# Performance work log

Hardware: AMD Instinct MI355X
Metric: run time of the kernel (lower is better)

Reference implementation:

```python
import jax, jax.numpy as jnp
import numpy as np
from jax import lax

V, E, H, K, T, B = 32000, 512, 512, 32, 256, 64
PAD_W = 0          # word_dict['PAD']
START, END, PAD_L = 30, 31, 0   # label_dict
NEG = -100000.0


def setup_inputs() -> dict:
    key = jax.random.key(0)
    ks = jax.random.split(key, 12)
    s = 1.0 / np.sqrt(H)
    tokens = jax.random.randint(ks[0], (T, B), 1, V, dtype=jnp.int32)   # >PAD_W -> mask all ones
    tags = jax.random.randint(ks[1], (T, B), 1, K - 2, dtype=jnp.int32)
    lengths = jnp.full((B,), T, dtype=jnp.int32)
    embed = jax.random.normal(ks[2], (V, E), jnp.float32) * 0.1
    wih0 = jax.random.uniform(ks[3], (2, 4 * H, E), jnp.float32, -s, s)
    whh0 = jax.random.uniform(ks[4], (2, 4 * H, H), jnp.float32, -s, s)
    b0 = jax.random.uniform(ks[5], (2, 4 * H), jnp.float32, -s, s)
    wih1 = jax.random.uniform(ks[6], (2, 4 * H, 2 * H), jnp.float32, -s, s)
    whh1 = jax.random.uniform(ks[7], (2, 4 * H, H), jnp.float32, -s, s)
    b1 = jax.random.uniform(ks[8], (2, 4 * H), jnp.float32, -s, s)
    lin_w = jax.random.uniform(ks[9], (K, 2 * H), jnp.float32, -s, s)
    lin_b = jax.random.uniform(ks[10], (K,), jnp.float32, -s, s)
    trans = jax.random.normal(ks[11], (K, K), jnp.float32)
    # replicate the torch transition init (same order of assignments)
    trans = trans.at[START, :].set(NEG)
    trans = trans.at[:, END].set(NEG)
    trans = trans.at[:, PAD_L].set(NEG)
    trans = trans.at[PAD_L, :].set(NEG)
    trans = trans.at[PAD_L, END].set(0.0)
    trans = trans.at[PAD_L, PAD_L].set(0.0)
    return dict(tokens=tokens, tags=tags, lengths=lengths, embed=embed,
                wih0=wih0, whh0=whh0, b0=b0, wih1=wih1, whh1=whh1, b1=b1,
                lin_w=lin_w, lin_b=lin_b, trans=trans)


def _lstm_dir(x, w_ih, w_hh, b, reverse):
    # x: [T,B,in] -> hs: [T,B,H]; gates precomputed as one big GEMM
    xp = jnp.einsum('tbi,gi->tbg', x, w_ih) + b  # [T,B,4H]
    h0 = jnp.zeros((x.shape[1], H), x.dtype)

    def step(carry, g_in):
        h, c = carry
        g = g_in + h @ w_hh.T
        i, f, gg, o = jnp.split(g, 4, axis=-1)  # torch gate order i,f,g,o
        c = jax.nn.sigmoid(f) * c + jax.nn.sigmoid(i) * jnp.tanh(gg)
        h = jax.nn.sigmoid(o) * jnp.tanh(c)
        return (h, c), h

    _, hs = lax.scan(step, (h0, h0), xp, reverse=reverse)
    return hs


def _bilstm_layer(x, wih, whh, b):
    return jnp.concatenate([_lstm_dir(x, wih[0], whh[0], b[0], False),
                            _lstm_dir(x, wih[1], whh[1], b[1], True)], axis=-1)


def reference(tokens, tags, lengths, embed, wih0, whh0, b0, wih1, whh1, b1,
              lin_w, lin_b, trans):
    mask = (tokens > PAD_W).astype(jnp.float32)  # [T,B]
    x = embed[tokens]                            # [T,B,E]
    x = _bilstm_layer(x, wih0, whh0, b0)
    x = _bilstm_layer(x, wih1, whh1, b1)
    feats = x @ lin_w.T + lin_b                  # [T,B,K]

    nB = tokens.shape[1]
    # ---- CRF forward algorithm: log Z(x) ----
    init = jnp.full((nB, K), NEG, feats.dtype).at[:, START].set(0.0)

    def step(score, inp):
        emit, m = inp  # [B,K], [B]
        # new[b,k] = logsumexp_j(score[b,j] + trans[k,j]) + emit[b,k]
        new = jax.nn.logsumexp(score[:, None, :] + trans[None, :, :], axis=2) + emit
        return jnp.where(m[:, None] > 0, new, score), None

    z, _ = lax.scan(step, init, (feats, mask))
    log_z = jax.nn.logsumexp(z + trans[END][None, :], axis=1)  # [B]

    # ---- gold path score (vectorized, masked deltas sum) ----
    start_row = jnp.full((1, nB), START, dtype=tags.dtype)
    te = jnp.concatenate([start_row, tags], axis=0)            # [T+1,B]
    trans_s = trans[te[1:], te[:-1]]                           # [T,B]
    emit_s = jnp.take_along_axis(feats, te[1:][..., None].astype(jnp.int32), axis=2)[..., 0]
    gold = jnp.sum(mask * (trans_s + emit_s), axis=0) + trans[END, te[-1]]

    return jnp.sum((log_z - gold) / lengths.astype(jnp.float32))
```

## Files before the change

kernel.cpp:

```cpp
#include <hip/hip_runtime.h>
#include <math.h>

#define T_STEPS 256
#define BATCH   64
#define HID     512
#define KTAGS   32
#define NEGV    -100000.0f
#define START_TAG 30
#define END_TAG   31

#define NBLK      256
#define SPIN_LIM  (1 << 26)
#define LAYER_DONE  300u
#define POISON_DONE 301u
#define POISON    0xFFFFFFFFFFFFFFFFULL

typedef __attribute__((ext_vector_type(8))) short short8;
typedef __attribute__((ext_vector_type(4))) float f32x4;

union V16 { uint4 u; short8 s; };
union HQ  { unsigned long long q[2]; short8 s; };

static __device__ __forceinline__ unsigned short f2b(float f) {
    unsigned u = __float_as_uint(f);
    return (unsigned short)((u + 0x7fffu + ((u >> 16) & 1u)) >> 16);
}
static __device__ __forceinline__ float b2f(unsigned short us) {
    return __uint_as_float(((unsigned)us) << 16);
}

__global__ __launch_bounds__(256) void init_zero(unsigned int* __restrict__ flags,
                                                 unsigned long long* __restrict__ hbuf,
                                                 float* __restrict__ out)
{
    int i = blockIdx.x * 256 + threadIdx.x;
    if (i < 131072)
        __hip_atomic_store(hbuf + i, POISON, __ATOMIC_RELAXED, __HIP_MEMORY_SCOPE_AGENT);
    if (i < 16384)
        __hip_atomic_store(flags + i, 0u, __ATOMIC_RELAXED, __HIP_MEMORY_SCOPE_AGENT);
    if (i == 0)
        __hip_atomic_store(out, 0.0f, __ATOMIC_RELAXED, __HIP_MEMORY_SCOPE_AGENT);
}

__global__ __launch_bounds__(256) void convert_embed(const float* __restrict__ src,
                                                     unsigned short* __restrict__ dst)
{
    long long i = ((long long)blockIdx.x * 256 + threadIdx.x) * 4;
    if (i >= (long long)32000 * 512) return;
    float4 v = *(const float4*)(src + i);
    ushort4 o;
    o.x = f2b(v.x); o.y = f2b(v.y); o.z = f2b(v.z); o.w = f2b(v.w);
    *(ushort4*)(dst + i) = o;
}

__global__ __launch_bounds__(256) void pack_w(const float* __restrict__ wih,
                                              const float* __restrict__ whh,
                                              int xK,
                                              unsigned short* __restrict__ wpack)
{
    const int xKt = xK >> 5, KT = xKt + 16;
    long long t = (long long)blockIdx.x * 256 + threadIdx.x;
    if (t >= (long long)2 * 64 * KT * 2 * 64) return;
    int lane = (int)(t & 63);
    long long rest = t >> 6;
    int nf = (int)(rest & 1); rest >>= 1;
    int kt = (int)(rest % KT); rest /= KT;
    int nt = (int)(rest % 64);
    int d  = (int)(rest / 64);
    int c = lane & 15, q = lane >> 4;
    int bc = nf * 16 + c;
    int r = (bc >> 3) * 512 + nt * 8 + (bc & 7);
    const float* src;
    if (kt < xKt) src = wih + ((long long)d * 2048 * xK + (long long)r * xK + kt * 32 + q * 8);
    else          src = whh + ((long long)d * 2048 * 512 + (long long)r * 512 + (kt - xKt) * 32 + q * 8);
    float4 v0 = *(const float4*)src;
    float4 v1 = *(const float4*)(src + 4);
    unsigned short o[8] = { f2b(v0.x), f2b(v0.y), f2b(v0.z), f2b(v0.w),
                            f2b(v1.x), f2b(v1.y), f2b(v1.z), f2b(v1.w) };
    *(uint4*)(wpack + t * 8) = *(const uint4*)o;
}

template<int XK>
static __device__ __forceinline__ void layer_steps(
    const int d, const int bg, const int nt, const int tid,
    const int* __restrict__ tokens,
    const unsigned short* __restrict__ embB,
    const unsigned short* __restrict__ hs_in,
    const unsigned short* __restrict__ wp,
    const float* __restrict__ bia,
    unsigned short* __restrict__ hso,
    unsigned long long* __restrict__ hbuf64,
    uint4* __restrict__ wldsH,
    float (&Gred)[4][32][33],
    int* __restrict__ tok_s)
{
    constexpr bool L0  = (XK == 512);
    constexpr int  xKt = XK >> 5;
    constexpr int  nX  = xKt >> 2;

    const int w = tid >> 6, lane = tid & 63;
    const int lm = lane & 15, q = lane >> 4;
    const int brow = tid >> 3, hc = tid & 7;

    const uint4* wp4 = (const uint4*)wp;
    for (int j = tid; j < 2048; j += 256)
        wldsH[j] = wp4[xKt * 128 + j];

    float breg[4];
    #pragma unroll
    for (int g = 0; g < 4; ++g) breg[g] = bia[g * 512 + nt * 8 + hc];
    float creg = 0.0f;

    __syncthreads();

    for (int s = 0; s < T_STEPS; ++s) {
        const int tt = d ? (T_STEPS - 1 - s) : s;

        if (L0 && tid < 32) tok_s[tid] = tokens[tt * BATCH + bg * 32 + tid];
        __syncthreads();

        const unsigned short* xr[2];
        #pragma unroll
        for (int mt = 0; mt < 2; ++mt) {
            int m = mt * 16 + lm;
            if (L0) xr[mt] = embB + (long long)tok_s[m] * 512;
            else    xr[mt] = hs_in + ((long long)tt * 64 + bg * 32 + m) * 1024;
        }

        uint4 av[nX][2], bv[nX][2];
        #pragma unroll
        for (int i = 0; i < nX; ++i) {
            const int kt = w * nX + i;
            #pragma unroll
            for (int mt = 0; mt < 2; ++mt)
                av[i][mt] = *(const uint4*)(xr[mt] + kt * 32 + q * 8);
            #pragma unroll
            for (int nf = 0; nf < 2; ++nf)
                bv[i][nf] = *(const uint4*)(wp + ((long long)kt * 128 + nf * 64 + lane) * 8);
        }

        HQ hq[4][2];
        const unsigned long long* hbq =
            hbuf64 + (long long)(((((s - 1) & 7) * 2 + d) * 2 + bg)) * 4096;
        if (s > 0) {
            #pragma unroll
            for (int i = 0; i < 4; ++i) {
                const int kth = w * 4 + i;
                #pragma unroll
                for (int mt = 0; mt < 2; ++mt) {
                    const int base = (kth * 4 + q) * 64 + (mt * 16 + lm) * 2;
                    hq[i][mt].q[0] = __hip_atomic_load(hbq + base,     __ATOMIC_RELAXED, __HIP_MEMORY_SCOPE_AGENT);
                    hq[i][mt].q[1] = __hip_atomic_load(hbq + base + 1, __ATOMIC_RELAXED, __HIP_MEMORY_SCOPE_AGENT);
                }
            }
        }

        f32x4 acc[2][2];
        #pragma unroll
        for (int mt = 0; mt < 2; ++mt)
            #pragma unroll
            for (int nf = 0; nf < 2; ++nf) acc[mt][nf] = (f32x4)0.0f;

        #pragma unroll
        for (int i = 0; i < nX; ++i) {
            V16 a0, a1, b0, b1;
            a0.u = av[i][0]; a1.u = av[i][1];
            b0.u = bv[i][0]; b1.u = bv[i][1];
            acc[0][0] = __builtin_amdgcn_mfma_f32_16x16x32_bf16(a0.s, b0.s, acc[0][0], 0, 0, 0);
            acc[0][1] = __builtin_amdgcn_mfma_f32_16x16x32_bf16(a0.s, b1.s, acc[0][1], 0, 0, 0);
            acc[1][0] = __builtin_amdgcn_mfma_f32_16x16x32_bf16(a1.s, b0.s, acc[1][0], 0, 0, 0);
            acc[1][1] = __builtin_amdgcn_mfma_f32_16x16x32_bf16(a1.s, b1.s, acc[1][1], 0, 0, 0);
        }

        if (s > 0) {
            int n = 0;
            for (;;) {
                int bad = 0;
                #pragma unroll
                for (int i = 0; i < 4; ++i) {
                    const int kth = w * 4 + i;
                    #pragma unroll
                    for (int mt = 0; mt < 2; ++mt) {
                        const int base = (kth * 4 + q) * 64 + (mt * 16 + lm) * 2;
                        if (hq[i][mt].q[0] == POISON) {
                            hq[i][mt].q[0] = __hip_atomic_load(hbq + base,     __ATOMIC_RELAXED, __HIP_MEMORY_SCOPE_AGENT);
                            bad = 1;
                        }
                        if (hq[i][mt].q[1] == POISON) {
                            hq[i][mt].q[1] = __hip_atomic_load(hbq + base + 1, __ATOMIC_RELAXED, __HIP_MEMORY_SCOPE_AGENT);
                            bad = 1;
                        }
                    }
                }
                if (!bad) break;
                __builtin_amdgcn_s_sleep(1);
                if (++n > SPIN_LIM) break;
            }

            #pragma unroll
            for (int i = 0; i < 4; ++i) {
                const int kth = w * 4 + i;
                V16 b0, b1;
                b0.u = wldsH[(kth * 2 + 0) * 64 + lane];
                b1.u = wldsH[(kth * 2 + 1) * 64 + lane];
                acc[0][0] = __builtin_amdgcn_mfma_f32_16x16x32_bf16(hq[i][0].s, b0.s, acc[0][0], 0, 0, 0);
                acc[0][1] = __builtin_amdgcn_mfma_f32_16x16x32_bf16(hq[i][0].s, b1.s, acc[0][1], 0, 0, 0);
                acc[1][0] = __builtin_amdgcn_mfma_f32_16x16x32_bf16(hq[i][1].s, b0.s, acc[1][0], 0, 0, 0);
                acc[1][1] = __builtin_amdgcn_mfma_f32_16x16x32_bf16(hq[i][1].s, b1.s, acc[1][1], 0, 0, 0);
            }
        }

        #pragma unroll
        for (int mt = 0; mt < 2; ++mt)
            #pragma unroll
            for (int nf = 0; nf < 2; ++nf)
                #pragma unroll
                for (int r = 0; r < 4; ++r)
                    Gred[w][nf * 16 + lm][mt * 16 + q * 4 + r] = acc[mt][nf][r];
        __syncthreads();

        float vg[4];
        #pragma unroll
        for (int g = 0; g < 4; ++g) {
            float v = breg[g];
            #pragma unroll
            for (int ww = 0; ww < 4; ++ww) v += Gred[ww][g * 8 + hc][brow];
            vg[g] = v;
        }
        const float si = 1.0f / (1.0f + __expf(-vg[0]));
        const float sf = 1.0f / (1.0f + __expf(-vg[1]));
        const float so = 1.0f / (1.0f + __expf(-vg[3]));
        const float cn = sf * creg + si * tanhf(vg[2]);
        const float hn = so * tanhf(cn);
        creg = cn;

        unsigned pv = (unsigned)f2b(hn);
        unsigned p2 = pv | (__shfl_xor(pv, 1) << 16);
        unsigned long long hv = (unsigned long long)p2
                              | ((unsigned long long)__shfl_xor(p2, 2) << 32);
        if ((tid & 3) == 0) {
            const int row = brow, cq = hc >> 2;
            unsigned long long* dst =
                hbuf64 + ((long long)((((s & 7) * 2 + d) * 2 + bg) * 64 + nt)) * 64 + row * 2 + cq;
            __hip_atomic_store(dst, hv, __ATOMIC_RELAXED, __HIP_MEMORY_SCOPE_AGENT);
            *(unsigned long long*)(hso + ((long long)tt * 64 + bg * 32 + row) * 1024
                                       + d * 512 + nt * 8 + cq * 4) = hv;
            unsigned long long* pdst =
                hbuf64 + ((long long)(((((s + 2) & 7) * 2 + d) * 2 + bg) * 64 + nt)) * 64 + row * 2 + cq;
            __hip_atomic_store(pdst, POISON, __ATOMIC_RELAXED, __HIP_MEMORY_SCOPE_AGENT);
        }
    }
}

__global__ __launch_bounds__(256, 1) void lstm_mfma(
    const int* __restrict__ tokens,
    const unsigned short* __restrict__ embB,
    const unsigned short* __restrict__ wp0,
    const unsigned short* __restrict__ wp1,
    const float* __restrict__ bb0, const float* __restrict__ bb1,
    unsigned short* __restrict__ hs0,
    unsigned short* __restrict__ hs1,
    unsigned long long* __restrict__ hbuf64,
    unsigned int* __restrict__ flags)
{
    __shared__ uint4 wldsH[2048];
    __shared__ float Gred[4][32][33];
    __shared__ int   tok_s[32];

    const int bid = blockIdx.x;
    const int d   = bid >> 7;
    const int bg  = (bid >> 6) & 1;
    const int nt  = bid & 63;
    const int tid = threadIdx.x;

    layer_steps<512>(d, bg, nt, tid, tokens, embB, (const unsigned short*)nullptr,
                     wp0 + (long long)(d * 64 + nt) * 32 * 1024,
                     bb0 + (long long)d * 2048,
                     hs0, hbuf64, wldsH, Gred, tok_s);

    {
        __threadfence();
        __syncthreads();
        if (tid == 0)
            __hip_atomic_store(flags + bid * 32, LAYER_DONE,
                               __ATOMIC_RELAXED, __HIP_MEMORY_SCOPE_AGENT);
        if (tid < 64) {
            int n = 0;
            for (;;) {
                unsigned a = __hip_atomic_load(flags + tid * 32,         __ATOMIC_RELAXED, __HIP_MEMORY_SCOPE_AGENT);
                unsigned b = __hip_atomic_load(flags + (tid + 64) * 32,  __ATOMIC_RELAXED, __HIP_MEMORY_SCOPE_AGENT);
                unsigned c = __hip_atomic_load(flags + (tid + 128) * 32, __ATOMIC_RELAXED, __HIP_MEMORY_SCOPE_AGENT);
                unsigned e = __hip_atomic_load(flags + (tid + 192) * 32, __ATOMIC_RELAXED, __HIP_MEMORY_SCOPE_AGENT);
                if (__all(a >= LAYER_DONE && b >= LAYER_DONE &&
                          c >= LAYER_DONE && e >= LAYER_DONE)) break;
                __builtin_amdgcn_s_sleep(1);
                if (++n > SPIN_LIM) break;
            }
        }
        __syncthreads();
        if (tid < 64) {
            #pragma unroll
            for (int p = 0; p < 8; ++p) {
                unsigned long long* pd =
                    hbuf64 + ((long long)(((p * 2 + d) * 2 + bg) * 64 + nt)) * 64 + tid;
                __hip_atomic_store(pd, POISON, __ATOMIC_RELAXED, __HIP_MEMORY_SCOPE_AGENT);
            }
        }
        asm volatile("s_waitcnt vmcnt(0)" ::: "memory");
        __syncthreads();
        if (tid == 0)
            __hip_atomic_store(flags + bid * 32, POISON_DONE,
                               __ATOMIC_RELAXED, __HIP_MEMORY_SCOPE_AGENT);
        if (tid < 64) {
            int n = 0;
            for (;;) {
                unsigned a = __hip_atomic_load(flags + tid * 32,         __ATOMIC_RELAXED, __HIP_MEMORY_SCOPE_AGENT);
                unsigned b = __hip_atomic_load(flags + (tid + 64) * 32,  __ATOMIC_RELAXED, __HIP_MEMORY_SCOPE_AGENT);
                unsigned c = __hip_atomic_load(flags + (tid + 128) * 32, __ATOMIC_RELAXED, __HIP_MEMORY_SCOPE_AGENT);
                unsigned e = __hip_atomic_load(flags + (tid + 192) * 32, __ATOMIC_RELAXED, __HIP_MEMORY_SCOPE_AGENT);
                if (__all(a >= POISON_DONE && b >= POISON_DONE &&
                          c >= POISON_DONE && e >= POISON_DONE)) break;
                __builtin_amdgcn_s_sleep(1);
                if (++n > SPIN_LIM) break;
            }
        }
        __syncthreads();
        __threadfence();
    }

    layer_steps<1024>(d, bg, nt, tid, tokens, embB, hs0,
                      wp1 + (long long)(d * 64 + nt) * 48 * 1024,
                      bb1 + (long long)d * 2048,
                      hs1, hbuf64, wldsH, Gred, tok_s);
}

__global__ __launch_bounds__(256) void gemm_feats(
    const unsigned short* __restrict__ A,
    const float* __restrict__ W,
    const float* __restrict__ bias,
    float* __restrict__ C,
    int M, int N, int K)
{
    __shared__ __align__(16) float As[64][34];
    __shared__ __align__(16) float Ws[32][68];

    const int m0 = blockIdx.y * 64;
    const int tid = threadIdx.x;
    const int tr = tid >> 4;
    const int tc = tid & 15;

    float acc[4][4];
    #pragma unroll
    for (int i = 0; i < 4; ++i)
        #pragma unroll
        for (int j = 0; j < 4; ++j) acc[i][j] = 0.0f;

    for (int k0 = 0; k0 < K; k0 += 32) {
        {
            int row = tid >> 2, g8 = tid & 3;
            uint4 v = *(const uint4*)(A + ((long long)(m0 + row)) * 1024 + k0 + g8 * 8);
            const unsigned short* pv = (const unsigned short*)&v;
            #pragma unroll
            for (int e = 0; e < 8; ++e) As[row][g8 * 8 + e] = b2f(pv[e]);
        }
        {
            int row = tid >> 3, q2 = tid & 7;
            float4 v = *(const float4*)(W + (long long)row * K + k0 + 4 * q2);
            Ws[4*q2+0][row] = v.x; Ws[4*q2+1][row] = v.y;
            Ws[4*q2+2][row] = v.z; Ws[4*q2+3][row] = v.w;
        }
        __syncthreads();
        #pragma unroll 8
        for (int kk = 0; kk < 32; ++kk) {
            float a0 = As[4*tr+0][kk], a1 = As[4*tr+1][kk];
            float a2 = As[4*tr+2][kk], a3 = As[4*tr+3][kk];
            float4 wv = *(const float4*)&Ws[kk][4*tc];
            acc[0][0] += a0*wv.x; acc[0][1] += a0*wv.y; acc[0][2] += a0*wv.z; acc[0][3] += a0*wv.w;
            acc[1][0] += a1*wv.x; acc[1][1] += a1*wv.y; acc[1][2] += a1*wv.z; acc[1][3] += a1*wv.w;
            acc[2][0] += a2*wv.x; acc[2][1] += a2*wv.y; acc[2][2] += a2*wv.z; acc[2][3] += a2*wv.w;
            acc[3][0] += a3*wv.x; acc[3][1] += a3*wv.y; acc[3][2] += a3*wv.z; acc[3][3] += a3*wv.w;
        }
        __syncthreads();
    }
    #pragma unroll
    for (int i = 0; i < 4; ++i) {
        int m = m0 + 4*tr + i;
        #pragma unroll
        for (int j = 0; j < 4; ++j) {
            int n = 4*tc + j;
            if (n < N) C[(long long)m * N + n] = acc[i][j] + bias[n];
        }
    }
}

__global__ __launch_bounds__(1024) void crf_kernel(
    const float* __restrict__ feats,
    const float* __restrict__ trans,
    const int*   __restrict__ tokens,
    const int*   __restrict__ tags,
    const int*   __restrict__ lengths,
    float* __restrict__ out)
{
    const int b = blockIdx.x;
    const int tid = threadIdx.x;
    __shared__ float tr_s[KTAGS*KTAGS];
    __shared__ float score_s[KTAGS];
    __shared__ float emit_s[KTAGS];
    __shared__ float red_s[16];
    __shared__ float logz_s;

    tr_s[tid] = trans[tid];
    if (tid < KTAGS) score_s[tid] = (tid == START_TAG) ? 0.0f : NEGV;
    __syncthreads();

    const int i = tid >> 5, j = tid & 31;
    for (int t = 0; t < T_STEPS; ++t) {
        if (tid < KTAGS) emit_s[tid] = feats[((long long)t*BATCH + b)*KTAGS + tid];
        __syncthreads();
        float e = score_s[j] + tr_s[i*KTAGS + j];
        float m = e;
        m = fmaxf(m, __shfl_xor(m, 1));  m = fmaxf(m, __shfl_xor(m, 2));
        m = fmaxf(m, __shfl_xor(m, 4));  m = fmaxf(m, __shfl_xor(m, 8));
        m = fmaxf(m, __shfl_xor(m, 16));
        float p = __expf(e - m);
        p += __shfl_xor(p, 1); p += __shfl_xor(p, 2); p += __shfl_xor(p, 4);
        p += __shfl_xor(p, 8); p += __shfl_xor(p, 16);
        float nv = m + __logf(p) + emit_s[i];
        int msk = tokens[(long long)t*BATCH + b] > 0;
        __syncthreads();
        if (j == 0) score_s[i] = msk ? nv : score_s[i];
        __syncthreads();
    }

    if (tid < KTAGS) {
        float v = score_s[tid] + tr_s[END_TAG*KTAGS + tid];
        float m = v;
        m = fmaxf(m, __shfl_xor(m, 1));  m = fmaxf(m, __shfl_xor(m, 2));
        m = fmaxf(m, __shfl_xor(m, 4));  m = fmaxf(m, __shfl_xor(m, 8));
        m = fmaxf(m, __shfl_xor(m, 16));
        float p = __expf(v - m);
        p += __shfl_xor(p, 1); p += __shfl_xor(p, 2); p += __shfl_xor(p, 4);
        p += __shfl_xor(p, 8); p += __shfl_xor(p, 16);
        if (tid == 0) logz_s = m + __logf(p);
    }
    __syncthreads();

    float val = 0.0f;
    if (tid < T_STEPS) {
        int t = tid;
        int cur  = tags[(long long)t*BATCH + b];
        int prev = (t == 0) ? START_TAG : tags[(long long)(t-1)*BATCH + b];
        int msk  = tokens[(long long)t*BATCH + b] > 0;
        if (msk) val = tr_s[cur*KTAGS + prev]
                     + feats[((long long)t*BATCH + b)*KTAGS + cur];
    }
    val += __shfl_xor(val, 1);  val += __shfl_xor(val, 2);
    val += __shfl_xor(val, 4);  val += __shfl_xor(val, 8);
    val += __shfl_xor(val, 16); val += __shfl_xor(val, 32);
    int wave = tid >> 6, lane = tid & 63;
    if (lane == 0) red_s[wave] = val;
    __syncthreads();
    if (tid == 0) {
        float g = 0.0f;
        #pragma unroll
        for (int w = 0; w < 16; ++w) g += red_s[w];
        g += tr_s[END_TAG*KTAGS + tags[(long long)(T_STEPS-1)*BATCH + b]];
        atomicAdd(out, (logz_s - g) / (float)lengths[b]);
    }
}

extern "C" void kernel_launch(void* const* d_in, const int* in_sizes, int n_in,
                              void* d_out, int out_size, void* d_ws, size_t ws_size,
                              hipStream_t stream) {
    const int*   tokens  = (const int*)  d_in[0];
    const int*   tags    = (const int*)  d_in[1];
    const int*   lengths = (const int*)  d_in[2];
    const float* embed   = (const float*)d_in[3];
    const float* wih0    = (const float*)d_in[4];
    const float* whh0    = (const float*)d_in[5];
    const float* b0      = (const float*)d_in[6];
    const float* wih1    = (const float*)d_in[7];
    const float* whh1    = (const float*)d_in[8];
    const float* b1      = (const float*)d_in[9];
    const float* lin_w   = (const float*)d_in[10];
    const float* lin_b   = (const float*)d_in[11];
    const float* trans   = (const float*)d_in[12];

    char* ws = (char*)d_ws;
    unsigned short* hs0   = (unsigned short*)(ws);
    unsigned short* hs1   = (unsigned short*)(ws +  33554432ULL);
    unsigned short* embB  = (unsigned short*)(ws +  67108864ULL);
    unsigned short* wp0   = (unsigned short*)(ws +  99876864ULL);
    unsigned short* wp1   = (unsigned short*)(ws + 108265472ULL);
    float*          feats = (float*)        (ws + 120848384ULL);
    unsigned int*   flagsP = (unsigned int*)feats;
    unsigned long long* hbufP = (unsigned long long*)((char*)feats + 65536);

    float* out = (float*)d_out;

    init_zero<<<dim3(512), 256, 0, stream>>>(flagsP, hbufP, out);
    convert_embed<<<dim3(16000), 256, 0, stream>>>(embed, embB);
    pack_w<<<dim3(2048), 256, 0, stream>>>(wih0, whh0, 512,  wp0);
    pack_w<<<dim3(3072), 256, 0, stream>>>(wih1, whh1, 1024, wp1);

    lstm_mfma<<<dim3(NBLK), 256, 0, stream>>>(
        tokens, embB, wp0, wp1, b0, b1, hs0, hs1, hbufP, flagsP);

    gemm_feats<<<dim3(1, 256, 1), 256, 0, stream>>>(
        hs1, lin_w, lin_b, feats, T_STEPS*BATCH, KTAGS, 2*HID);

    crf_kernel<<<dim3(BATCH), 1024, 0, stream>>>(feats, trans, tokens, tags,
                                                 lengths, out);
}
```

Measured before the change: 2.424 ms.

## Keep input-projection weights in LDS and wait per k-tile on hidden state

The full packed weight slice, both the input-projection and the recurrent parts, is now loaded into LDS once per layer. Previously the input-projection part was re-read from global memory every timestep. The poll loop for the previous step's hidden state now waits and runs the MFMAs one k-tile at a time instead of waiting for all tiles first, so compute can start on whatever data has already arrived. The cost is a larger LDS footprint, 96KB of weights plus the reduction buffer, and more LDS read traffic per step.

```diff
diff --git a/kernel.cpp b/kernel.cpp
--- a/kernel.cpp
+++ b/kernel.cpp
@@ -90,12 +90,13 @@
     const float* __restrict__ bia,
     unsigned short* __restrict__ hso,
     unsigned long long* __restrict__ hbuf64,
-    uint4* __restrict__ wldsH,
+    uint4* __restrict__ wlds,
     float (&Gred)[4][32][33],
     int* __restrict__ tok_s)
 {
     constexpr bool L0  = (XK == 512);
     constexpr int  xKt = XK >> 5;
+    constexpr int  KT  = xKt + 16;
     constexpr int  nX  = xKt >> 2;
 
     const int w = tid >> 6, lane = tid & 63;
@@ -103,8 +104,8 @@
     const int brow = tid >> 3, hc = tid & 7;
 
     const uint4* wp4 = (const uint4*)wp;
-    for (int j = tid; j < 2048; j += 256)
-        wldsH[j] = wp4[xKt * 128 + j];
+    for (int j = tid; j < KT * 128; j += 256)
+        wlds[j] = wp4[j];
 
     float breg[4];
     #pragma unroll
@@ -127,16 +128,13 @@
             else    xr[mt] = hs_in + ((long long)tt * 64 + bg * 32 + m) * 1024;
         }
 
-        uint4 av[nX][2], bv[nX][2];
+        uint4 av[nX][2];
         #pragma unroll
         for (int i = 0; i < nX; ++i) {
             const int kt = w * nX + i;
             #pragma unroll
             for (int mt = 0; mt < 2; ++mt)
                 av[i][mt] = *(const uint4*)(xr[mt] + kt * 32 + q * 8);
-            #pragma unroll
-            for (int nf = 0; nf < 2; ++nf)
-                bv[i][nf] = *(const uint4*)(wp + ((long long)kt * 128 + nf * 64 + lane) * 8);
         }
 
         HQ hq[4][2];
@@ -163,9 +161,11 @@
 
         #pragma unroll
         for (int i = 0; i < nX; ++i) {
+            const int kt = w * nX + i;
             V16 a0, a1, b0, b1;
             a0.u = av[i][0]; a1.u = av[i][1];
-            b0.u = bv[i][0]; b1.u = bv[i][1];
+            b0.u = wlds[(kt * 2 + 0) * 64 + lane];
+            b1.u = wlds[(kt * 2 + 1) * 64 + lane];
             acc[0][0] = __builtin_amdgcn_mfma_f32_16x16x32_bf16(a0.s, b0.s, acc[0][0], 0, 0, 0);
             acc[0][1] = __builtin_amdgcn_mfma_f32_16x16x32_bf16(a0.s, b1.s, acc[0][1], 0, 0, 0);
             acc[1][0] = __builtin_amdgcn_mfma_f32_16x16x32_bf16(a1.s, b0.s, acc[1][0], 0, 0, 0);
@@ -173,12 +173,12 @@
         }
 
         if (s > 0) {
-            int n = 0;
-            for (;;) {
-                int bad = 0;
-                #pragma unroll
-                for (int i = 0; i < 4; ++i) {
-                    const int kth = w * 4 + i;
+            #pragma unroll
+            for (int i = 0; i < 4; ++i) {
+                const int kth = w * 4 + i;
+                int n = 0;
+                for (;;) {
+                    int bad = 0;
                     #pragma unroll
                     for (int mt = 0; mt < 2; ++mt) {
                         const int base = (kth * 4 + q) * 64 + (mt * 16 + lm) * 2;
@@ -191,18 +191,13 @@
                             bad = 1;
                         }
                     }
+                    if (!bad) break;
+                    __builtin_amdgcn_s_sleep(1);
+                    if (++n > SPIN_LIM) break;
                 }
-                if (!bad) break;
-                __builtin_amdgcn_s_sleep(1);
-                if (++n > SPIN_LIM) break;
-            }
-
-            #pragma unroll
-            for (int i = 0; i < 4; ++i) {
-                const int kth = w * 4 + i;
                 V16 b0, b1;
-                b0.u = wldsH[(kth * 2 + 0) * 64 + lane];
-                b1.u = wldsH[(kth * 2 + 1) * 64 + lane];
+                b0.u = wlds[((xKt + kth) * 2 + 0) * 64 + lane];
+                b1.u = wlds[((xKt + kth) * 2 + 1) * 64 + lane];
                 acc[0][0] = __builtin_amdgcn_mfma_f32_16x16x32_bf16(hq[i][0].s, b0.s, acc[0][0], 0, 0, 0);
                 acc[0][1] = __builtin_amdgcn_mfma_f32_16x16x32_bf16(hq[i][0].s, b1.s, acc[0][1], 0, 0, 0);
                 acc[1][0] = __builtin_amdgcn_mfma_f32_16x16x32_bf16(hq[i][1].s, b0.s, acc[1][0], 0, 0, 0);
@@ -263,7 +258,7 @@
     unsigned long long* __restrict__ hbuf64,
     unsigned int* __restrict__ flags)
 {
-    __shared__ uint4 wldsH[2048];
+    __shared__ uint4 wlds[6144];
     __shared__ float Gred[4][32][33];
     __shared__ int   tok_s[32];
 
@@ -276,7 +271,7 @@
     layer_steps<512>(d, bg, nt, tid, tokens, embB, (const unsigned short*)nullptr,
                      wp0 + (long long)(d * 64 + nt) * 32 * 1024,
                      bb0 + (long long)d * 2048,
-                     hs0, hbuf64, wldsH, Gred, tok_s);
+                     hs0, hbuf64, wlds, Gred, tok_s);
 
     {
         __threadfence();
@@ -331,7 +326,7 @@
     layer_steps<1024>(d, bg, nt, tid, tokens, embB, hs0,
                       wp1 + (long long)(d * 64 + nt) * 48 * 1024,
                       bb1 + (long long)d * 2048,
-                      hs1, hbuf64, wldsH, Gred, tok_s);
+                      hs1, hbuf64, wlds, Gred, tok_s);
 }
 
 __global__ __launch_bounds__(256) void gemm_feats(
```

Result: slower. 2.483 ms (+2.4%).
